# Optimization experiments

Measured on AMD Instinct MI355X. Metric: run time of the kernel, lower is better.

## Reference

```python
import jax, jax.numpy as jnp
import numpy as np

D_MODEL = 1024
NUM_HEADS = 16
D_HEAD = D_MODEL // NUM_HEADS


def setup_inputs() -> dict:
    key = jax.random.key(0)
    ks = jax.random.split(key, 12)
    B, S = 2, 2048
    scale = 1.0 / np.sqrt(D_MODEL)
    inp = {
        "q": jax.random.normal(ks[0], (B, S, D_MODEL), jnp.float32),
        "k": jax.random.normal(ks[1], (B, S, D_MODEL), jnp.float32),
        "v": jax.random.normal(ks[2], (B, S, D_MODEL), jnp.float32),
        # per-head projection weights stacked: [H, d_model, d_head]
        "Wq": jax.random.normal(ks[3], (NUM_HEADS, D_MODEL, D_HEAD), jnp.float32) * scale,
        "bq": jax.random.normal(ks[4], (NUM_HEADS, D_HEAD), jnp.float32) * scale,
        "Wk": jax.random.normal(ks[5], (NUM_HEADS, D_MODEL, D_HEAD), jnp.float32) * scale,
        "bk": jax.random.normal(ks[6], (NUM_HEADS, D_HEAD), jnp.float32) * scale,
        "Wv": jax.random.normal(ks[7], (NUM_HEADS, D_MODEL, D_HEAD), jnp.float32) * scale,
        "bv": jax.random.normal(ks[8], (NUM_HEADS, D_HEAD), jnp.float32) * scale,
        "Wo": jax.random.normal(ks[9], (D_MODEL, D_MODEL), jnp.float32) * scale,
        "bo": jax.random.normal(ks[10], (D_MODEL,), jnp.float32) * scale,
    }
    return inp


def reference(q, k, v, Wq, bq, Wk, bk, Wv, bv, Wo, bo):
    # Per-head linear projections, batched over heads: [b,s,d] x [h,d,e] -> [b,h,s,e]
    qh = jnp.einsum("bsd,hde->bhse", q, Wq) + bq[None, :, None, :]
    kh = jnp.einsum("bsd,hde->bhse", k, Wk) + bk[None, :, None, :]
    vh = jnp.einsum("bsd,hde->bhse", v, Wv) + bv[None, :, None, :]
    # Scaled dot-product attention per head
    scores = jnp.einsum("bhse,bhte->bhst", qh, kh) / jnp.sqrt(jnp.asarray(D_HEAD, qh.dtype))
    weights = jax.nn.softmax(scores, axis=-1)
    out = jnp.einsum("bhst,bhte->bhse", weights, vh)
    # Concatenate heads along feature dim (head order preserved), then output linear
    B, H, S, E = out.shape
    out = out.transpose(0, 2, 1, 3).reshape(B, S, H * E)
    return out @ Wo + bo
```

## Files before the change

### kernel.cpp

```cpp
#include <hip/hip_runtime.h>
#include <cstdint>
#include <math.h>


typedef __bf16 bf16;
typedef __bf16 bf16x2 __attribute__((ext_vector_type(2)));
typedef __bf16 bf16x4 __attribute__((ext_vector_type(4)));
typedef __bf16 bf16x8 __attribute__((ext_vector_type(8)));
typedef float f32x4 __attribute__((ext_vector_type(4)));
typedef float f32x16 __attribute__((ext_vector_type(16)));
typedef unsigned u32x4 __attribute__((ext_vector_type(4)));

__device__ __forceinline__ void gl2lds16(const void* g, void* l) {
  __builtin_amdgcn_global_load_lds(
      (const __attribute__((address_space(1))) unsigned int*)g,
      (__attribute__((address_space(3))) unsigned int*)l,
      16, 0, 0);
}

__device__ __forceinline__ unsigned pkbf(float a, float b) {
  bf16x2 t;
  t[0] = (bf16)a;
  t[1] = (bf16)b;
  return __builtin_bit_cast(unsigned, t);
}

__global__ __launch_bounds__(256) void k_cvt_all(const float* __restrict__ q,
                                                 const float* __restrict__ k,
                                                 const float* __restrict__ v,
                                                 const float* __restrict__ Wq,
                                                 const float* __restrict__ Wk,
                                                 const float* __restrict__ Wv,
                                                 const float* __restrict__ Wo,
                                                 bf16* __restrict__ qkv,
                                                 bf16* __restrict__ WT,
                                                 bf16* __restrict__ WoT) {
  __shared__ float tl[64][65];
  const int bid = blockIdx.x;
  const int t = threadIdx.x;
  if (bid < 12288) {
    const int by = bid >> 12, bx = bid & 4095;
    const float* in = by == 0 ? q : (by == 1 ? k : v);
    bf16* out = qkv + (size_t)by * 4194304;
    const size_t i = ((size_t)bx * 256 + t) * 4;
    const float4 vv = *(const float4*)(in + i);
    bf16x4 o;
    o[0] = (bf16)vv.x; o[1] = (bf16)vv.y; o[2] = (bf16)vv.z; o[3] = (bf16)vv.w;
    *(bf16x4*)(out + i) = o;
  } else if (bid < 13056) {
    const int wb = bid - 12288;
    const int sel = wb >> 8;
    const int rem = wb & 255;
    const int h = rem >> 4;
    const int d0 = (rem & 15) << 6;
    const float* W = sel == 0 ? Wq : (sel == 1 ? Wk : Wv);
    const int r = t >> 2;
    const float* srcp = W + (size_t)h * 65536 + (size_t)(d0 + r) * 64 + (t & 3) * 4;
#pragma unroll
    for (int j = 0; j < 4; ++j) {
      const float4 vv = *(const float4*)(srcp + j * 16);
      const int c = (t & 3) * 4 + j * 16;
      tl[r][c] = vv.x; tl[r][c + 1] = vv.y; tl[r][c + 2] = vv.z; tl[r][c + 3] = vv.w;
    }
    __syncthreads();
    bf16* dst = WT + (size_t)sel * 1048576;
#pragma unroll
    for (int pass = 0; pass < 2; ++pass) {
      const int e = (t >> 3) + pass * 32;
      const int dd = (t & 7) * 8;
      bf16x8 o;
#pragma unroll
      for (int j = 0; j < 8; ++j) o[j] = (bf16)tl[dd + j][e];
      *(bf16x8*)(dst + (size_t)(h * 64 + e) * 1024 + d0 + dd) = o;
    }
  } else {
    const int wb = bid - 13056;
    const int n0 = (wb >> 4) << 6;
    const int k0 = (wb & 15) << 6;
    const int r = t >> 2;
    const float* srcp = Wo + (size_t)(k0 + r) * 1024 + n0 + (t & 3) * 4;
#pragma unroll
    for (int j = 0; j < 4; ++j) {
      const float4 vv = *(const float4*)(srcp + j * 16);
      const int c = (t & 3) * 4 + j * 16;
      tl[r][c] = vv.x; tl[r][c + 1] = vv.y; tl[r][c + 2] = vv.z; tl[r][c + 3] = vv.w;
    }
    __syncthreads();
#pragma unroll
    for (int pass = 0; pass < 2; ++pass) {
      const int e = (t >> 3) + pass * 32;
      const int dd = (t & 7) * 8;
      bf16x8 o;
#pragma unroll
      for (int j = 0; j < 8; ++j) o[j] = (bf16)tl[dd + j][e];
      *(bf16x8*)(WoT + (size_t)(n0 + e) * 1024 + k0 + dd) = o;
    }
  }
}

__global__ __launch_bounds__(512, 4) void k_gemm_qkv(const bf16* __restrict__ Abase,
                                                     const bf16* __restrict__ Bt,
                                                     const float* __restrict__ bq,
                                                     const float* __restrict__ bk,
                                                     const float* __restrict__ bv,
                                                     bf16* __restrict__ Qh,
                                                     bf16* __restrict__ Kh,
                                                     bf16* __restrict__ Vt) {
  __shared__ __align__(16) bf16 lds[32768];
  const int t = threadIdx.x;
  const int lane = t & 63;
  const int lane15 = lane & 15;
  const int quad = lane >> 4;
  const int w = t >> 6;
  const int wm = w >> 2;
  const int wn = w & 3;

  const int bid = blockIdx.x;
  const int wgid = (bid & 7) * 96 + (bid >> 3);
  const int nb = wgid % 24;
  const int mb = wgid / 24;
  const int sel = nb >> 3;
  const int nbl = (nb & 7) << 7;

  const bf16* A = Abase + (size_t)sel * 4194304;
  const int sr = t >> 3;
  const int sc = ((t & 7) - sr) & 7;
  const bf16* AgS = A + (size_t)(mb * 128 + sr) * 1024 + sc * 8;
  const bf16* BgS = Bt + (size_t)(nb * 128 + sr) * 1024 + sc * 8;

#define QKV_STAGE(kt, d)                           \
  do {                                             \
    const int _k = (kt) * 64;                      \
    bf16* _la = lds + (d) * 8192 + t * 8;          \
    bf16* _lb = lds + 16384 + (d) * 8192 + t * 8;  \
    gl2lds16(AgS + _k, _la);                       \
    gl2lds16(AgS + 65536 + _k, _la + 4096);        \
    gl2lds16(BgS + _k, _lb);                       \
    gl2lds16(BgS + 65536 + _k, _lb + 4096);        \
  } while (0)

  f32x4 acc[4][2] = {};
  const int arow = (wm * 64 + lane15) * 64;
  const int brow = 16384 + (wn * 32 + lane15) * 64;

  QKV_STAGE(0, 0);
  QKV_STAGE(1, 1);

#pragma unroll 2
  for (int kt = 0; kt < 16; ++kt) {
    const int d = kt & 1;
    if (kt == 15)
      asm volatile("s_waitcnt vmcnt(0)" ::: "memory");
    else
      asm volatile("s_waitcnt vmcnt(4)" ::: "memory");
    __builtin_amdgcn_s_barrier();
    const int base = d * 8192;
    {
      const int p = ((quad + lane15) & 7) * 8;
      bf16x8 af[4], bfr[2];
#pragma unroll
      for (int i = 0; i < 4; ++i)
        af[i] = *(const bf16x8*)(lds + base + arow + i * 1024 + p);
#pragma unroll
      for (int j = 0; j < 2; ++j)
        bfr[j] = *(const bf16x8*)(lds + base + brow + j * 1024 + p);
      __builtin_amdgcn_s_setprio(1);
#pragma unroll
      for (int i = 0; i < 4; ++i)
#pragma unroll
        for (int j = 0; j < 2; ++j)
          acc[i][j] = __builtin_amdgcn_mfma_f32_16x16x32_bf16(af[i], bfr[j], acc[i][j], 0, 0, 0);
      __builtin_amdgcn_s_setprio(0);
    }
    {
      const int p = ((quad + 4 + lane15) & 7) * 8;
      bf16x8 ag[4], bg[2];
#pragma unroll
      for (int i = 0; i < 4; ++i)
        ag[i] = *(const bf16x8*)(lds + base + arow + i * 1024 + p);
#pragma unroll
      for (int j = 0; j < 2; ++j)
        bg[j] = *(const bf16x8*)(lds + base + brow + j * 1024 + p);
      asm volatile("s_waitcnt lgkmcnt(0)" ::: "memory");
      __builtin_amdgcn_s_barrier();
      if (kt < 14) QKV_STAGE(kt + 2, d);
      __builtin_amdgcn_s_setprio(1);
#pragma unroll
      for (int i = 0; i < 4; ++i)
#pragma unroll
        for (int j = 0; j < 2; ++j)
          acc[i][j] = __builtin_amdgcn_mfma_f32_16x16x32_bf16(ag[i], bg[j], acc[i][j], 0, 0, 0);
      __builtin_amdgcn_s_setprio(0);
    }
  }
#undef QKV_STAGE

  const float scale = sel == 0 ? 0.18033688011112042f : 1.0f;
  const float* bias = sel == 0 ? bq : (sel == 1 ? bk : bv);
  const int mbase = mb * 128 + wm * 64;
  if (sel < 2) {
    bf16* outp = sel == 0 ? Qh : Kh;
#pragma unroll
    for (int j = 0; j < 2; ++j) {
      const int n = nbl + wn * 32 + j * 16 + lane15;
      const float bvl = bias[n];
      const int h = n >> 6, e = n & 63;
#pragma unroll
      for (int i = 0; i < 4; ++i) {
#pragma unroll
        for (int r = 0; r < 4; ++r) {
          const int m = mbase + i * 16 + quad * 4 + r;
          const float vv = (acc[i][j][r] + bvl) * scale;
          const int b = m >> 11, s = m & 2047;
          outp[(size_t)(b * 16 + h) * 131072 + s * 64 + e] = (bf16)vv;
        }
      }
    }
  } else {
#pragma unroll
    for (int j = 0; j < 2; ++j) {
      const int n = nbl + wn * 32 + j * 16 + lane15;
      const float bvl = bias[n];
      const int h = n >> 6, e = n & 63;
#pragma unroll
      for (int i = 0; i < 4; ++i) {
        const int m = mbase + i * 16 + quad * 4;
        const int b = m >> 11, s = m & 2047;
        bf16x4 o;
#pragma unroll
        for (int r = 0; r < 4; ++r) o[r] = (bf16)(acc[i][j][r] + bvl);
        *(bf16x4*)(Vt + (size_t)(b * 16 + h) * 131072 + e * 2048 + s) = o;
      }
    }
  }
}

__global__ __launch_bounds__(512, 4) void k_attn(const bf16* __restrict__ Qh,
                                                 const bf16* __restrict__ Kh,
                                                 const bf16* __restrict__ Vt,
                                                 bf16* __restrict__ attn) {
  __shared__ __align__(16) bf16 lds[32768];
  const int t = threadIdx.x;
  const int w = t >> 6;
  const int lane = t & 63;
  const int lane31 = lane & 31;
  const int hi = lane >> 5;

  const int bid = blockIdx.x;
  const int xcd = bid & 7;
  const int loc = bid >> 3;
  const int bh = xcd * 4 + (loc >> 4);
  const int qt = loc & 15;

  const bf16* Qp = Qh + (size_t)bh * 131072;
  const bf16* Kp = Kh + (size_t)bh * 131072;
  const bf16* Vp = Vt + (size_t)bh * 131072;
  const int h = w >> 2;
  const int q0 = qt * 128 + (w & 3) * 32;

  bf16x8 aq[4];
#pragma unroll
  for (int kc = 0; kc < 4; ++kc)
    aq[kc] = *(const bf16x8*)(Qp + (size_t)(q0 + lane31) * 64 + kc * 16 + hi * 8);

  int raddr[4];
#pragma unroll
  for (int cc = 0; cc < 4; ++cc)
    raddr[cc] = lane31 * 64 + (((cc * 2 + hi + lane31) & 7) << 3);

  const bf16* kg[2];
  const bf16* vg[2];
  int kdst[2], vdst[2];
#pragma unroll
  for (int i = 0; i < 2; ++i) {
    const int cid = w * 2 + i;
    const int half = cid >> 3;
    const int sl = ((cid & 7) << 6) + lane;
    const int row = sl >> 3;
    const int c = ((sl & 7) - row) & 7;
    kg[i] = Kp + ((size_t)(half << 10) + row) * 64 + c * 8;
    vg[i] = Vp + (size_t)row * 2048 + (half << 10) + c * 8;
    kdst[i] = (half << 14) + ((cid & 7) << 9);
    vdst[i] = kdst[i] + 8192;
  }

#define ATTN_STAGE(it)                                          \
  do {                                                          \
    const int _po = ((it) & 1) << 12;                           \
    gl2lds16(kg[0] + (size_t)(it) * 4096, lds + kdst[0] + _po); \
    gl2lds16(vg[0] + (it) * 64, lds + vdst[0] + _po);           \
    gl2lds16(kg[1] + (size_t)(it) * 4096, lds + kdst[1] + _po); \
    gl2lds16(vg[1] + (it) * 64, lds + vdst[1] + _po);           \
  } while (0)

  f32x16 O[2] = {};
  float l_ = 0.f;

  ATTN_STAGE(0);
  ATTN_STAGE(1);

#pragma unroll 2
  for (int it = 0; it < 16; ++it) {
    const int bufo = (it & 1) << 12;
    if (it == 15)
      asm volatile("s_waitcnt vmcnt(0)" ::: "memory");
    else
      asm volatile("s_waitcnt vmcnt(4)" ::: "memory");
    __builtin_amdgcn_s_barrier();

    const bf16* Kl = lds + (h << 14) + bufo;
    f32x16 sa = {}, sb = {};
#pragma unroll
    for (int kc = 0; kc < 4; ++kc) {
      bf16x8 a0 = *(const bf16x8*)(Kl + raddr[kc]);
      bf16x8 a1 = *(const bf16x8*)(Kl + 2048 + raddr[kc]);
      sa = __builtin_amdgcn_mfma_f32_32x32x16_bf16(a0, aq[kc], sa, 0, 0, 0);
      sb = __builtin_amdgcn_mfma_f32_32x32x16_bf16(a1, aq[kc], sb, 0, 0, 0);
    }

    float rs = 0.f;
#pragma unroll
    for (int r = 0; r < 16; ++r) {
      sa[r] = __builtin_amdgcn_exp2f(sa[r]);
      sb[r] = __builtin_amdgcn_exp2f(sb[r]);
      rs += sa[r] + sb[r];
    }
    rs += __shfl_xor(rs, 32);
    l_ += rs;

    unsigned P2[2][8];
#pragma unroll
    for (int kq = 0; kq < 8; ++kq) {
      P2[0][kq] = pkbf(sa[2 * kq], sa[2 * kq + 1]);
      P2[1][kq] = pkbf(sb[2 * kq], sb[2 * kq + 1]);
    }

    const bf16* Vl = lds + (h << 14) + 8192 + bufo;
#pragma unroll
    for (int kk = 0; kk < 4; ++kk) {
      const int kmt = kk >> 1, kc = kk & 1;
      const unsigned mineA = hi ? P2[kmt][4 * kc + 2] : P2[kmt][4 * kc];
      const unsigned mineB = hi ? P2[kmt][4 * kc + 3] : P2[kmt][4 * kc + 1];
      const unsigned sendA = hi ? P2[kmt][4 * kc] : P2[kmt][4 * kc + 2];
      const unsigned sendB = hi ? P2[kmt][4 * kc + 1] : P2[kmt][4 * kc + 3];
      const unsigned ZA = (unsigned)__shfl_xor((int)sendA, 32);
      const unsigned ZB = (unsigned)__shfl_xor((int)sendB, 32);
      u32x4 bpi;
      bpi[0] = hi ? ZA : mineA;
      bpi[1] = hi ? ZB : mineB;
      bpi[2] = hi ? mineA : ZA;
      bpi[3] = hi ? mineB : ZB;
      const bf16x8 bp = __builtin_bit_cast(bf16x8, bpi);
#pragma unroll
      for (int emt = 0; emt < 2; ++emt) {
        bf16x8 av = *(const bf16x8*)(Vl + emt * 2048 + raddr[kk]);
        O[emt] = __builtin_amdgcn_mfma_f32_32x32x16_bf16(av, bp, O[emt], 0, 0, 0);
      }
    }

    asm volatile("s_waitcnt lgkmcnt(0)" ::: "memory");
    __builtin_amdgcn_s_barrier();
    if (it < 14) ATTN_STAGE(it + 2);
  }
#undef ATTN_STAGE

  float* fl = (float*)lds;
  __syncthreads();
  if (w >= 4) {
#pragma unroll
    for (int emt = 0; emt < 2; ++emt)
#pragma unroll
      for (int r = 0; r < 16; ++r)
        fl[(w - 4) * 2048 + (emt * 16 + r) * 64 + lane] = O[emt][r];
    if (lane < 32) fl[8192 + (w - 4) * 32 + lane] = l_;
  }
  __syncthreads();
  if (w < 4) {
#pragma unroll
    for (int emt = 0; emt < 2; ++emt)
#pragma unroll
      for (int r = 0; r < 16; ++r)
        O[emt][r] += fl[w * 2048 + (emt * 16 + r) * 64 + lane];
    const float lsum = l_ + fl[8192 + w * 32 + lane31];
    const float inv = 1.0f / lsum;

    const int b = bh >> 4, hh = bh & 15;
    const int q = q0 + lane31;
    bf16* orow = attn + (size_t)(b * 2048 + q) * 1024 + hh * 64;
#pragma unroll
    for (int emt = 0; emt < 2; ++emt) {
#pragma unroll
      for (int kp = 0; kp < 8; ++kp) {
        const int r = 2 * kp;
        const int e0 = emt * 32 + (r & 3) + 8 * (kp >> 1) + 4 * hi;
        bf16x2 pr;
        pr[0] = (bf16)(O[emt][r] * inv);
        pr[1] = (bf16)(O[emt][r + 1] * inv);
        *(bf16x2*)(orow + e0) = pr;
      }
    }
  }
}

__global__ __launch_bounds__(512, 4) void k_gemm2(const bf16* __restrict__ A,
                                                  const bf16* __restrict__ Bt,
                                                  const float* __restrict__ bias,
                                                  float* __restrict__ outp) {
  __shared__ __align__(16) bf16 lds[32768];
  const int t = threadIdx.x;
  const int lane = t & 63;
  const int lane15 = lane & 15;
  const int quad = lane >> 4;
  const int w = t >> 6;
  const int wm = w >> 2;
  const int wn = w & 3;

  const int bid = blockIdx.x;
  const int wgid = (bid & 7) * 32 + (bid >> 3);
  const int nb = wgid & 7;
  const int mb = wgid >> 3;

  const int sr = t >> 3;
  const int sc = ((t & 7) - sr) & 7;
  const bf16* AgS = A + (size_t)(mb * 128 + sr) * 1024 + sc * 8;
  const bf16* BgS = Bt + (size_t)(nb * 128 + sr) * 1024 + sc * 8;

#define G2_STAGE(kt, d)                            \
  do {                                             \
    const int _k = (kt) * 64;                      \
    bf16* _la = lds + (d) * 8192 + t * 8;          \
    bf16* _lb = lds + 16384 + (d) * 8192 + t * 8;  \
    gl2lds16(AgS + _k, _la);                       \
    gl2lds16(AgS + 65536 + _k, _la + 4096);        \
    gl2lds16(BgS + _k, _lb);                       \
    gl2lds16(BgS + 65536 + _k, _lb + 4096);        \
  } while (0)

  f32x4 acc[4][2] = {};
  const int arow = (wm * 64 + lane15) * 64;
  const int brow = 16384 + (wn * 32 + lane15) * 64;

  G2_STAGE(0, 0);
  G2_STAGE(1, 1);

#pragma unroll 2
  for (int kt = 0; kt < 16; ++kt) {
    const int d = kt & 1;
    if (kt == 15)
      asm volatile("s_waitcnt vmcnt(0)" ::: "memory");
    else
      asm volatile("s_waitcnt vmcnt(4)" ::: "memory");
    __builtin_amdgcn_s_barrier();
    const int base = d * 8192;
    {
      const int p = ((quad + lane15) & 7) * 8;
      bf16x8 af[4], bfr[2];
#pragma unroll
      for (int i = 0; i < 4; ++i)
        af[i] = *(const bf16x8*)(lds + base + arow + i * 1024 + p);
#pragma unroll
      for (int j = 0; j < 2; ++j)
        bfr[j] = *(const bf16x8*)(lds + base + brow + j * 1024 + p);
      __builtin_amdgcn_s_setprio(1);
#pragma unroll
      for (int i = 0; i < 4; ++i)
#pragma unroll
        for (int j = 0; j < 2; ++j)
          acc[i][j] = __builtin_amdgcn_mfma_f32_16x16x32_bf16(af[i], bfr[j], acc[i][j], 0, 0, 0);
      __builtin_amdgcn_s_setprio(0);
    }
    {
      const int p = ((quad + 4 + lane15) & 7) * 8;
      bf16x8 ag[4], bg[2];
#pragma unroll
      for (int i = 0; i < 4; ++i)
        ag[i] = *(const bf16x8*)(lds + base + arow + i * 1024 + p);
#pragma unroll
      for (int j = 0; j < 2; ++j)
        bg[j] = *(const bf16x8*)(lds + base + brow + j * 1024 + p);
      asm volatile("s_waitcnt lgkmcnt(0)" ::: "memory");
      __builtin_amdgcn_s_barrier();
      if (kt < 14) G2_STAGE(kt + 2, d);
      __builtin_amdgcn_s_setprio(1);
#pragma unroll
      for (int i = 0; i < 4; ++i)
#pragma unroll
        for (int j = 0; j < 2; ++j)
          acc[i][j] = __builtin_amdgcn_mfma_f32_16x16x32_bf16(ag[i], bg[j], acc[i][j], 0, 0, 0);
      __builtin_amdgcn_s_setprio(0);
    }
  }
#undef G2_STAGE

  const int mbase = mb * 128 + wm * 64;
  const int nbase = nb * 128 + wn * 32;
#pragma unroll
  for (int j = 0; j < 2; ++j) {
    const int n = nbase + j * 16 + lane15;
    const float bv = bias[n];
#pragma unroll
    for (int i = 0; i < 4; ++i) {
#pragma unroll
      for (int r = 0; r < 4; ++r) {
        const int m = mbase + i * 16 + quad * 4 + r;
        outp[(size_t)m * 1024 + n] = acc[i][j][r] + bv;
      }
    }
  }
}

extern "C" void kernel_launch(void* const* d_in, const int* in_sizes, int n_in,
                              void* d_out, int out_size, void* d_ws, size_t ws_size,
                              hipStream_t stream) {
  (void)in_sizes; (void)n_in; (void)out_size; (void)ws_size;
  const float* q = (const float*)d_in[0];
  const float* k = (const float*)d_in[1];
  const float* v = (const float*)d_in[2];
  const float* Wq = (const float*)d_in[3];
  const float* bq = (const float*)d_in[4];
  const float* Wk = (const float*)d_in[5];
  const float* bk = (const float*)d_in[6];
  const float* Wv = (const float*)d_in[7];
  const float* bv = (const float*)d_in[8];
  const float* Wo = (const float*)d_in[9];
  const float* bo = (const float*)d_in[10];

  bf16* ws = (bf16*)d_ws;
  bf16* qkv = ws;
  bf16* WqkvT = qkv + 12582912;
  bf16* WoT = WqkvT + 3145728;
  bf16* Qh = WoT + 1048576;
  bf16* Kh = Qh + 4194304;
  bf16* Vt = Kh + 4194304;
  bf16* attnb = Vt + 4194304;

  k_cvt_all<<<13312, 256, 0, stream>>>(q, k, v, Wq, Wk, Wv, Wo, qkv, WqkvT, WoT);
  k_gemm_qkv<<<768, 512, 0, stream>>>(qkv, WqkvT, bq, bk, bv, Qh, Kh, Vt);
  k_attn<<<512, 512, 0, stream>>>(Qh, Kh, Vt, attnb);
  k_gemm2<<<256, 512, 0, stream>>>(attnb, WoT, bo, (float*)d_out);
}
```

Before: 211.8 us.

## Load K/V fragments directly from global into registers, dropping LDS staging

```diff
diff --git a/kernel.cpp b/kernel.cpp
--- a/kernel.cpp
+++ b/kernel.cpp
@@ -235,11 +235,11 @@
   }
 }
 
-__global__ __launch_bounds__(512, 4) void k_attn(const bf16* __restrict__ Qh,
+__global__ __launch_bounds__(512, 2) void k_attn(const bf16* __restrict__ Qh,
                                                  const bf16* __restrict__ Kh,
                                                  const bf16* __restrict__ Vt,
                                                  bf16* __restrict__ attn) {
-  __shared__ __align__(16) bf16 lds[32768];
+  __shared__ float fl[8320];
   const int t = threadIdx.x;
   const int w = t >> 6;
   const int lane = t & 63;
@@ -263,108 +263,87 @@
   for (int kc = 0; kc < 4; ++kc)
     aq[kc] = *(const bf16x8*)(Qp + (size_t)(q0 + lane31) * 64 + kc * 16 + hi * 8);
 
-  int raddr[4];
-#pragma unroll
-  for (int cc = 0; cc < 4; ++cc)
-    raddr[cc] = lane31 * 64 + (((cc * 2 + hi + lane31) & 7) << 3);
-
-  const bf16* kg[2];
-  const bf16* vg[2];
-  int kdst[2], vdst[2];
-#pragma unroll
-  for (int i = 0; i < 2; ++i) {
-    const int cid = w * 2 + i;
-    const int half = cid >> 3;
-    const int sl = ((cid & 7) << 6) + lane;
-    const int row = sl >> 3;
-    const int c = ((sl & 7) - row) & 7;
-    kg[i] = Kp + ((size_t)(half << 10) + row) * 64 + c * 8;
-    vg[i] = Vp + (size_t)row * 2048 + (half << 10) + c * 8;
-    kdst[i] = (half << 14) + ((cid & 7) << 9);
-    vdst[i] = kdst[i] + 8192;
-  }
-
-#define ATTN_STAGE(it)                                          \
-  do {                                                          \
-    const int _po = ((it) & 1) << 12;                           \
-    gl2lds16(kg[0] + (size_t)(it) * 4096, lds + kdst[0] + _po); \
-    gl2lds16(vg[0] + (it) * 64, lds + vdst[0] + _po);           \
-    gl2lds16(kg[1] + (size_t)(it) * 4096, lds + kdst[1] + _po); \
-    gl2lds16(vg[1] + (it) * 64, lds + vdst[1] + _po);           \
+  const bf16* Kbase = Kp + ((size_t)(h << 10) + lane31) * 64 + hi * 8;
+  const bf16* Vbase = Vp + (size_t)lane31 * 2048 + (h << 10) + hi * 8;
+
+  bf16x8 kfA[8], kfB[8], vf[8];
+
+#define LOADK(f, it)                                                   \
+  do {                                                                 \
+    const bf16* _b = Kbase + (size_t)(it) * 4096;                      \
+    _Pragma("unroll") for (int kc = 0; kc < 4; ++kc) {                 \
+      f[kc * 2] = *(const bf16x8*)(_b + kc * 16);                      \
+      f[kc * 2 + 1] = *(const bf16x8*)(_b + 2048 + kc * 16);           \
+    }                                                                  \
+  } while (0)
+
+#define LOADV(it)                                                      \
+  do {                                                                 \
+    const bf16* _b = Vbase + (it) * 64;                                \
+    _Pragma("unroll") for (int kk = 0; kk < 4; ++kk) {                 \
+      vf[kk * 2] = *(const bf16x8*)(_b + kk * 16);                     \
+      vf[kk * 2 + 1] = *(const bf16x8*)(_b + 65536 + kk * 16);         \
+    }                                                                  \
   } while (0)
 
   f32x16 O[2] = {};
   float l_ = 0.f;
 
-  ATTN_STAGE(0);
-  ATTN_STAGE(1);
-
-#pragma unroll 2
-  for (int it = 0; it < 16; ++it) {
-    const int bufo = (it & 1) << 12;
-    if (it == 15)
-      asm volatile("s_waitcnt vmcnt(0)" ::: "memory");
-    else
-      asm volatile("s_waitcnt vmcnt(4)" ::: "memory");
-    __builtin_amdgcn_s_barrier();
-
-    const bf16* Kl = lds + (h << 14) + bufo;
-    f32x16 sa = {}, sb = {};
-#pragma unroll
-    for (int kc = 0; kc < 4; ++kc) {
-      bf16x8 a0 = *(const bf16x8*)(Kl + raddr[kc]);
-      bf16x8 a1 = *(const bf16x8*)(Kl + 2048 + raddr[kc]);
-      sa = __builtin_amdgcn_mfma_f32_32x32x16_bf16(a0, aq[kc], sa, 0, 0, 0);
-      sb = __builtin_amdgcn_mfma_f32_32x32x16_bf16(a1, aq[kc], sb, 0, 0, 0);
-    }
-
-    float rs = 0.f;
-#pragma unroll
-    for (int r = 0; r < 16; ++r) {
-      sa[r] = __builtin_amdgcn_exp2f(sa[r]);
-      sb[r] = __builtin_amdgcn_exp2f(sb[r]);
-      rs += sa[r] + sb[r];
-    }
-    rs += __shfl_xor(rs, 32);
-    l_ += rs;
-
-    unsigned P2[2][8];
-#pragma unroll
-    for (int kq = 0; kq < 8; ++kq) {
-      P2[0][kq] = pkbf(sa[2 * kq], sa[2 * kq + 1]);
-      P2[1][kq] = pkbf(sb[2 * kq], sb[2 * kq + 1]);
-    }
-
-    const bf16* Vl = lds + (h << 14) + 8192 + bufo;
-#pragma unroll
-    for (int kk = 0; kk < 4; ++kk) {
-      const int kmt = kk >> 1, kc = kk & 1;
-      const unsigned mineA = hi ? P2[kmt][4 * kc + 2] : P2[kmt][4 * kc];
-      const unsigned mineB = hi ? P2[kmt][4 * kc + 3] : P2[kmt][4 * kc + 1];
-      const unsigned sendA = hi ? P2[kmt][4 * kc] : P2[kmt][4 * kc + 2];
-      const unsigned sendB = hi ? P2[kmt][4 * kc + 1] : P2[kmt][4 * kc + 3];
-      const unsigned ZA = (unsigned)__shfl_xor((int)sendA, 32);
-      const unsigned ZB = (unsigned)__shfl_xor((int)sendB, 32);
-      u32x4 bpi;
-      bpi[0] = hi ? ZA : mineA;
-      bpi[1] = hi ? ZB : mineB;
-      bpi[2] = hi ? mineA : ZA;
-      bpi[3] = hi ? mineB : ZB;
-      const bf16x8 bp = __builtin_bit_cast(bf16x8, bpi);
-#pragma unroll
-      for (int emt = 0; emt < 2; ++emt) {
-        bf16x8 av = *(const bf16x8*)(Vl + emt * 2048 + raddr[kk]);
-        O[emt] = __builtin_amdgcn_mfma_f32_32x32x16_bf16(av, bp, O[emt], 0, 0, 0);
-      }
-    }
-
-    asm volatile("s_waitcnt lgkmcnt(0)" ::: "memory");
-    __builtin_amdgcn_s_barrier();
-    if (it < 14) ATTN_STAGE(it + 2);
-  }
-#undef ATTN_STAGE
-
-  float* fl = (float*)lds;
+  LOADK(kfA, 0);
+
+#define ATTN_BODY(KF, KN, it)                                                     \
+  do {                                                                            \
+    LOADV(it);                                                                    \
+    f32x16 sa = {}, sb = {};                                                      \
+    __builtin_amdgcn_s_setprio(1);                                                \
+    _Pragma("unroll") for (int kc = 0; kc < 4; ++kc) {                            \
+      sa = __builtin_amdgcn_mfma_f32_32x32x16_bf16(KF[kc * 2], aq[kc], sa, 0, 0, 0);   \
+      sb = __builtin_amdgcn_mfma_f32_32x32x16_bf16(KF[kc * 2 + 1], aq[kc], sb, 0, 0, 0); \
+    }                                                                             \
+    __builtin_amdgcn_s_setprio(0);                                                \
+    if ((it) < 15) LOADK(KN, (it) + 1);                                           \
+    float rs = 0.f;                                                               \
+    _Pragma("unroll") for (int r = 0; r < 16; ++r) {                              \
+      sa[r] = __builtin_amdgcn_exp2f(sa[r]);                                      \
+      sb[r] = __builtin_amdgcn_exp2f(sb[r]);                                      \
+      rs += sa[r] + sb[r];                                                        \
+    }                                                                             \
+    rs += __shfl_xor(rs, 32);                                                     \
+    l_ += rs;                                                                     \
+    unsigned P2[2][8];                                                            \
+    _Pragma("unroll") for (int kq = 0; kq < 8; ++kq) {                            \
+      P2[0][kq] = pkbf(sa[2 * kq], sa[2 * kq + 1]);                               \
+      P2[1][kq] = pkbf(sb[2 * kq], sb[2 * kq + 1]);                               \
+    }                                                                             \
+    _Pragma("unroll") for (int kk = 0; kk < 4; ++kk) {                            \
+      const int kmt = kk >> 1, kc2 = kk & 1;                                      \
+      const unsigned mineA = hi ? P2[kmt][4 * kc2 + 2] : P2[kmt][4 * kc2];        \
+      const unsigned mineB = hi ? P2[kmt][4 * kc2 + 3] : P2[kmt][4 * kc2 + 1];    \
+      const unsigned sendA = hi ? P2[kmt][4 * kc2] : P2[kmt][4 * kc2 + 2];        \
+      const unsigned sendB = hi ? P2[kmt][4 * kc2 + 1] : P2[kmt][4 * kc2 + 3];    \
+      const unsigned ZA = (unsigned)__shfl_xor((int)sendA, 32);                   \
+      const unsigned ZB = (unsigned)__shfl_xor((int)sendB, 32);                   \
+      u32x4 bpi;                                                                  \
+      bpi[0] = hi ? ZA : mineA;                                                   \
+      bpi[1] = hi ? ZB : mineB;                                                   \
+      bpi[2] = hi ? mineA : ZA;                                                   \
+      bpi[3] = hi ? mineB : ZB;                                                   \
+      const bf16x8 bp = __builtin_bit_cast(bf16x8, bpi);                          \
+      __builtin_amdgcn_s_setprio(1);                                              \
+      O[0] = __builtin_amdgcn_mfma_f32_32x32x16_bf16(vf[kk * 2], bp, O[0], 0, 0, 0);   \
+      O[1] = __builtin_amdgcn_mfma_f32_32x32x16_bf16(vf[kk * 2 + 1], bp, O[1], 0, 0, 0); \
+      __builtin_amdgcn_s_setprio(0);                                              \
+    }                                                                             \
+  } while (0)
+
+  for (int it = 0; it < 16; it += 2) {
+    ATTN_BODY(kfA, kfB, it);
+    ATTN_BODY(kfB, kfA, it + 1);
+  }
+#undef ATTN_BODY
+#undef LOADK
+#undef LOADV
+
   __syncthreads();
   if (w >= 4) {
 #pragma unroll
```

After: 285.9 us. 1.35x slower.

## Software-pipeline attention loop: overlap next QK^T with current PV via triple-buffered K

Applied to the files above, without the earlier changes.

```diff
diff --git a/kernel.cpp b/kernel.cpp
--- a/kernel.cpp
+++ b/kernel.cpp
@@ -239,7 +239,7 @@
                                                  const bf16* __restrict__ Kh,
                                                  const bf16* __restrict__ Vt,
                                                  bf16* __restrict__ attn) {
-  __shared__ __align__(16) bf16 lds[32768];
+  __shared__ __align__(16) bf16 lds[40960];
   const int t = threadIdx.x;
   const int w = t >> 6;
   const int lane = t & 63;
@@ -256,6 +256,7 @@
   const bf16* Kp = Kh + (size_t)bh * 131072;
   const bf16* Vp = Vt + (size_t)bh * 131072;
   const int h = w >> 2;
+  const int hb = h * 20480;
   const int q0 = qt * 128 + (w & 3) * 32;
 
   bf16x8 aq[4];
@@ -280,36 +281,37 @@
     const int c = ((sl & 7) - row) & 7;
     kg[i] = Kp + ((size_t)(half << 10) + row) * 64 + c * 8;
     vg[i] = Vp + (size_t)row * 2048 + (half << 10) + c * 8;
-    kdst[i] = (half << 14) + ((cid & 7) << 9);
-    vdst[i] = kdst[i] + 8192;
-  }
-
-#define ATTN_STAGE(it)                                          \
-  do {                                                          \
-    const int _po = ((it) & 1) << 12;                           \
-    gl2lds16(kg[0] + (size_t)(it) * 4096, lds + kdst[0] + _po); \
-    gl2lds16(vg[0] + (it) * 64, lds + vdst[0] + _po);           \
-    gl2lds16(kg[1] + (size_t)(it) * 4096, lds + kdst[1] + _po); \
-    gl2lds16(vg[1] + (it) * 64, lds + vdst[1] + _po);           \
+    kdst[i] = half * 20480 + ((cid & 7) << 9);
+    vdst[i] = half * 20480 + 12288 + ((cid & 7) << 9);
+  }
+
+#define SKST(it, kb3)                                                  \
+  do {                                                                 \
+    gl2lds16(kg[0] + (size_t)(it) * 4096, lds + kdst[0] + (kb3) * 4096); \
+    gl2lds16(kg[1] + (size_t)(it) * 4096, lds + kdst[1] + (kb3) * 4096); \
+  } while (0)
+#define SVST(it)                                                       \
+  do {                                                                 \
+    gl2lds16(vg[0] + (it) * 64, lds + vdst[0] + ((it) & 1) * 4096);    \
+    gl2lds16(vg[1] + (it) * 64, lds + vdst[1] + ((it) & 1) * 4096);    \
   } while (0)
 
   f32x16 O[2] = {};
   float l_ = 0.f;
-
-  ATTN_STAGE(0);
-  ATTN_STAGE(1);
-
-#pragma unroll 2
-  for (int it = 0; it < 16; ++it) {
-    const int bufo = (it & 1) << 12;
-    if (it == 15)
-      asm volatile("s_waitcnt vmcnt(0)" ::: "memory");
-    else
-      asm volatile("s_waitcnt vmcnt(4)" ::: "memory");
-    __builtin_amdgcn_s_barrier();
-
-    const bf16* Kl = lds + (h << 14) + bufo;
+  unsigned P2A[2][8], P2B[2][8];
+
+  SKST(0, 0);
+  SVST(0);
+  SKST(1, 1);
+  SVST(1);
+  SKST(2, 2);
+  asm volatile("s_waitcnt vmcnt(8)" ::: "memory");
+  __builtin_amdgcn_s_barrier();
+
+  {
+    const bf16* Kl = lds + hb;
     f32x16 sa = {}, sb = {};
+    __builtin_amdgcn_s_setprio(1);
 #pragma unroll
     for (int kc = 0; kc < 4; ++kc) {
       bf16x8 a0 = *(const bf16x8*)(Kl + raddr[kc]);
@@ -317,7 +319,7 @@
       sa = __builtin_amdgcn_mfma_f32_32x32x16_bf16(a0, aq[kc], sa, 0, 0, 0);
       sb = __builtin_amdgcn_mfma_f32_32x32x16_bf16(a1, aq[kc], sb, 0, 0, 0);
     }
-
+    __builtin_amdgcn_s_setprio(0);
     float rs = 0.f;
 #pragma unroll
     for (int r = 0; r < 16; ++r) {
@@ -327,42 +329,92 @@
     }
     rs += __shfl_xor(rs, 32);
     l_ += rs;
-
-    unsigned P2[2][8];
 #pragma unroll
     for (int kq = 0; kq < 8; ++kq) {
-      P2[0][kq] = pkbf(sa[2 * kq], sa[2 * kq + 1]);
-      P2[1][kq] = pkbf(sb[2 * kq], sb[2 * kq + 1]);
-    }
-
-    const bf16* Vl = lds + (h << 14) + 8192 + bufo;
-#pragma unroll
-    for (int kk = 0; kk < 4; ++kk) {
-      const int kmt = kk >> 1, kc = kk & 1;
-      const unsigned mineA = hi ? P2[kmt][4 * kc + 2] : P2[kmt][4 * kc];
-      const unsigned mineB = hi ? P2[kmt][4 * kc + 3] : P2[kmt][4 * kc + 1];
-      const unsigned sendA = hi ? P2[kmt][4 * kc] : P2[kmt][4 * kc + 2];
-      const unsigned sendB = hi ? P2[kmt][4 * kc + 1] : P2[kmt][4 * kc + 3];
-      const unsigned ZA = (unsigned)__shfl_xor((int)sendA, 32);
-      const unsigned ZB = (unsigned)__shfl_xor((int)sendB, 32);
-      u32x4 bpi;
-      bpi[0] = hi ? ZA : mineA;
-      bpi[1] = hi ? ZB : mineB;
-      bpi[2] = hi ? mineA : ZA;
-      bpi[3] = hi ? mineB : ZB;
-      const bf16x8 bp = __builtin_bit_cast(bf16x8, bpi);
-#pragma unroll
-      for (int emt = 0; emt < 2; ++emt) {
-        bf16x8 av = *(const bf16x8*)(Vl + emt * 2048 + raddr[kk]);
-        O[emt] = __builtin_amdgcn_mfma_f32_32x32x16_bf16(av, bp, O[emt], 0, 0, 0);
-      }
-    }
-
-    asm volatile("s_waitcnt lgkmcnt(0)" ::: "memory");
-    __builtin_amdgcn_s_barrier();
-    if (it < 14) ATTN_STAGE(it + 2);
-  }
-#undef ATTN_STAGE
+      P2A[0][kq] = pkbf(sa[2 * kq], sa[2 * kq + 1]);
+      P2A[1][kq] = pkbf(sb[2 * kq], sb[2 * kq + 1]);
+    }
+  }
+
+  int kb = 0;
+
+#define ATTN_STEP(P2CUR, P2NXT, jj)                                               \
+  do {                                                                            \
+    if ((jj) == 15)                                                               \
+      asm volatile("s_waitcnt vmcnt(0)" ::: "memory");                            \
+    else if ((jj) == 14)                                                          \
+      asm volatile("s_waitcnt vmcnt(2)" ::: "memory");                            \
+    else                                                                          \
+      asm volatile("s_waitcnt vmcnt(4)" ::: "memory");                            \
+    __builtin_amdgcn_s_barrier();                                                 \
+    int krd = kb + 1;                                                             \
+    if (krd == 3) krd = 0;                                                        \
+    f32x16 sa = {}, sb = {};                                                      \
+    if ((jj) < 15) {                                                              \
+      const bf16* Kl = lds + hb + krd * 4096;                                     \
+      __builtin_amdgcn_s_setprio(1);                                              \
+      _Pragma("unroll") for (int kc = 0; kc < 4; ++kc) {                          \
+        bf16x8 a0 = *(const bf16x8*)(Kl + raddr[kc]);                             \
+        bf16x8 a1 = *(const bf16x8*)(Kl + 2048 + raddr[kc]);                      \
+        sa = __builtin_amdgcn_mfma_f32_32x32x16_bf16(a0, aq[kc], sa, 0, 0, 0);    \
+        sb = __builtin_amdgcn_mfma_f32_32x32x16_bf16(a1, aq[kc], sb, 0, 0, 0);    \
+      }                                                                           \
+      __builtin_amdgcn_s_setprio(0);                                              \
+    }                                                                             \
+               \
+    {                                                                             \
+      const bf16* Vl = lds + hb + 12288 + ((jj) & 1) * 4096;                      \
+      _Pragma("unroll") for (int kk = 0; kk < 4; ++kk) {                          \
+        const int kmt = kk >> 1, kc2 = kk & 1;                                    \
+        const unsigned mineA = hi ? P2CUR[kmt][4 * kc2 + 2] : P2CUR[kmt][4 * kc2];      \
+        const unsigned mineB = hi ? P2CUR[kmt][4 * kc2 + 3] : P2CUR[kmt][4 * kc2 + 1];  \
+        const unsigned sendA = hi ? P2CUR[kmt][4 * kc2] : P2CUR[kmt][4 * kc2 + 2];      \
+        const unsigned sendB = hi ? P2CUR[kmt][4 * kc2 + 1] : P2CUR[kmt][4 * kc2 + 3];  \
+        const unsigned ZA = (unsigned)__shfl_xor((int)sendA, 32);                 \
+        const unsigned ZB = (unsigned)__shfl_xor((int)sendB, 32);                 \
+        u32x4 bpi;                                                                \
+        bpi[0] = hi ? ZA : mineA;                                                 \
+        bpi[1] = hi ? ZB : mineB;                                                 \
+        bpi[2] = hi ? mineA : ZA;                                                 \
+        bpi[3] = hi ? mineB : ZB;                                                 \
+        const bf16x8 bp = __builtin_bit_cast(bf16x8, bpi);                        \
+        bf16x8 av0 = *(const bf16x8*)(Vl + raddr[kk]);                            \
+        bf16x8 av1 = *(const bf16x8*)(Vl + 2048 + raddr[kk]);                     \
+        __builtin_amdgcn_s_setprio(1);                                            \
+        O[0] = __builtin_amdgcn_mfma_f32_32x32x16_bf16(av0, bp, O[0], 0, 0, 0);   \
+        O[1] = __builtin_amdgcn_mfma_f32_32x32x16_bf16(av1, bp, O[1], 0, 0, 0);   \
+        __builtin_amdgcn_s_setprio(0);                                            \
+      }                                                                           \
+    }                                                                             \
+    asm volatile("s_waitcnt lgkmcnt(0)" ::: "memory");                            \
+    __builtin_amdgcn_s_barrier();                                                 \
+    if ((jj) <= 12) SKST((jj) + 3, kb);                                           \
+    if ((jj) <= 13) SVST((jj) + 2);                                               \
+        \
+    if ((jj) < 15) {                                                              \
+      float rs = 0.f;                                                             \
+      _Pragma("unroll") for (int r = 0; r < 16; ++r) {                            \
+        sa[r] = __builtin_amdgcn_exp2f(sa[r]);                                    \
+        sb[r] = __builtin_amdgcn_exp2f(sb[r]);                                    \
+        rs += sa[r] + sb[r];                                                      \
+      }                                                                           \
+      rs += __shfl_xor(rs, 32);                                                   \
+      l_ += rs;                                                                   \
+      _Pragma("unroll") for (int kq = 0; kq < 8; ++kq) {                          \
+        P2NXT[0][kq] = pkbf(sa[2 * kq], sa[2 * kq + 1]);                          \
+        P2NXT[1][kq] = pkbf(sb[2 * kq], sb[2 * kq + 1]);                          \
+      }                                                                           \
+    }                                                                             \
+    kb = krd;                                                                     \
+  } while (0)
+
+  for (int j = 0; j < 16; j += 2) {
+    ATTN_STEP(P2A, P2B, j);
+    ATTN_STEP(P2B, P2A, j + 1);
+  }
+#undef ATTN_STEP
+#undef SKST
+#undef SVST
 
   float* fl = (float*)lds;
   __syncthreads();
```

Measured after the change: 283.3 us. 33.7% more time.
